# Kernel optimization log

Measured on AMD Instinct MI355X. Metric: run time of the kernel, lower is better.

The kernel has to match this reference:

```python
import jax, jax.numpy as jnp
import numpy as np

# Lens/CCD constants from the source module
DX = 0.00859375
F = 8.0
OX = 5.5 / 2.0   # CCD_width / 2
OY = 7.7 / 2.0   # CCD_length / 2

B, C, H, W = 4, 3, 1024, 2048


def _make_bn(h, w):
    # bn[i, j] = floor((cos(atan(dx*(j-ox)/f)) - 1) * (i - oy)), as in __init__
    j = np.arange(w, dtype=np.float64)
    i = np.arange(h, dtype=np.float64)
    a0 = np.arctan(DX * (j - OX) / F)
    bn = np.floor((np.cos(a0)[None, :] - 1.0) * (i[:, None] - OY))
    return bn.astype(np.int32)


def setup_inputs() -> dict:
    key = jax.random.key(0)
    k1, k2 = jax.random.split(key)
    x = jax.random.normal(k1, (B, C, H, W), dtype=jnp.float32)
    # Conv2d(3, 3, kernel_size=3, bias=False) weight: (out_c, in_c, kh, kw)
    weight = jax.random.normal(k2, (3, 3, 3, 3), dtype=jnp.float32) * 0.1
    bn = jnp.asarray(_make_bn(H, W))  # int32 distortion LUT, shape (H, W)
    return {"x": x, "weight": weight, "bn": bn}


def reference(x, weight, bn):
    B_, C_, H_, W_ = x.shape
    Hi, Wj = H_ - 2, W_ // 2 - 2  # active region: i+2 < H and j+2 < W//2
    i = jnp.arange(Hi)
    j = jnp.arange(Wj)
    p = jnp.arange(3)  # k // 3 (patch row)
    q = jnp.arange(3)  # k % 3  (patch col)
    # column used for the LUT wraps for j >= 256 (j1 = j % 256)
    j1 = jnp.where(j >= 256, j % 256, j)
    rows = i[:, None] + p[None, :]        # (Hi, 3)
    cols = j1[:, None] + q[None, :]       # (Wj, 3)
    # tb(i, j, p, q) = i + p + bn[i + p, j1 + q]
    bn_sel = bn[rows[:, None, :, None], cols[None, :, None, :]]  # (Hi, Wj, 3, 3)
    R = rows[:, None, :, None] + bn_sel                          # source row indices
    # Faithful quirk from the source: patch column index into input is q (0..2),
    # NOT j + q: matrix1[:, :, p, q] = input[:, :, tb, q]
    gathered = x[:, :, R, q]  # (B, C, Hi, Wj, 3, 3)
    out_act = jnp.einsum('bcijpq,ocpq->boij', gathered, weight)  # per-pixel 3x3 conv
    # guard from the source: only write when i + 2 + bn[i+2, j+2] < H
    mask = (i[:, None] + 2 + bn[i[:, None] + 2, j[None, :] + 2]) < H_
    out_act = out_act * mask.astype(out_act.dtype)
    return jnp.zeros((B_, C_, H_, W_), x.dtype).at[:, :, :Hi, :Wj].set(out_act)
```

## Files before the change

kernel.cpp:

```cpp
#include <hip/hip_runtime.h>


#define HH 1024
#define WW 2048
#define HI 1022
#define WJ 1022

__global__ __launch_bounds__(256, 4) void dis_conv_kernel(
    const float* __restrict__ x,
    const float* __restrict__ w,
    const int*   __restrict__ bn,
    float*       __restrict__ out)
{
    const int bi = blockIdx.x;
    const int b  = bi >> 10;
    const int i  = bi & 1023;
    const int t  = threadIdx.x;

    __shared__ __align__(16) float v[3][256];
    __shared__ __align__(16) float mask_s[1024];

    const bool activeRow = (i < HI);

    float acc0 = 0.f, acc1 = 0.f, acc2 = 0.f;
    if (activeRow) {
        const int jm = t;
        #pragma unroll
        for (int p = 0; p < 3; ++p) {
            const int r = i + p;
            const int* bnrow = bn + (size_t)r * WW;
            #pragma unroll
            for (int q = 0; q < 3; ++q) {
                int Rv = r + bnrow[jm + q];
                if (Rv < 0) Rv += HH;
                const float* xp = x + ((size_t)b * 3) * HH * WW + (size_t)Rv * WW + q;
                #pragma unroll
                for (int c = 0; c < 3; ++c) {
                    const float xv = xp[(size_t)c * HH * WW];
                    acc0 += xv * w[ 0 + c * 9 + p * 3 + q];
                    acc1 += xv * w[27 + c * 9 + p * 3 + q];
                    acc2 += xv * w[54 + c * 9 + p * 3 + q];
                }
            }
        }
    }
    v[0][t] = acc0;
    v[1][t] = acc1;
    v[2][t] = acc2;

    #pragma unroll
    for (int jj = 0; jj < 4; ++jj) {
        const int j = t + jj * 256;
        float m = 0.f;
        if (activeRow && j < WJ) {
            m = ((i + 2) + bn[(size_t)(i + 2) * WW + (j + 2)] < HH) ? 1.f : 0.f;
        }
        mask_s[j] = m;
    }
    __syncthreads();

    #pragma unroll
    for (int o = 0; o < 3; ++o) {
        float* orow = out + (((size_t)b * 3 + o) * HH + i) * WW;
        #pragma unroll
        for (int it = 0; it < 2; ++it) {
            const int j4 = (t + it * 256) * 4;
            float4 val;
            if (j4 < 1024) {
                const float4 vv = *(const float4*)&v[o][j4 & 255];
                const float4 mm = *(const float4*)&mask_s[j4];
                val = make_float4(vv.x * mm.x, vv.y * mm.y, vv.z * mm.z, vv.w * mm.w);
            } else {
                val = make_float4(0.f, 0.f, 0.f, 0.f);
            }
            *(float4*)&orow[j4] = val;
        }
    }
}

extern "C" void kernel_launch(void* const* d_in, const int* in_sizes, int n_in,
                              void* d_out, int out_size, void* d_ws, size_t ws_size,
                              hipStream_t stream) {
    const float* x   = (const float*)d_in[0];
    const float* w   = (const float*)d_in[1];
    const int*   bn  = (const int*)d_in[2];
    float*       out = (float*)d_out;

    dis_conv_kernel<<<dim3(4096), dim3(256), 0, stream>>>(x, w, bn, out);
}
```

Measured before the change: 176.7 us.

## Split into compute and write kernels, sharing LUT indices across batch

Computes the 256 distinct column values per row once in a first kernel that loads the bn LUT once and reuses it across all four batches, storing results and the mask in workspace. A second kernel then streams the masked values and zeros into the output with float4 stores. This removes the redundant per-batch bn reads and mask computation. In exchange it adds a second launch and a workspace round trip, and the compute kernel runs only 1022 blocks.

```diff
diff --git a/kernel.cpp b/kernel.cpp
--- a/kernel.cpp
+++ b/kernel.cpp
@@ -6,74 +6,102 @@
 #define HI 1022
 #define WJ 1022
 
-__global__ __launch_bounds__(256, 4) void dis_conv_kernel(
+#define VWS_FLOATS (12 * 1024 * 256)
+
+__global__ __launch_bounds__(256) void compute_v_kernel(
     const float* __restrict__ x,
     const float* __restrict__ w,
     const int*   __restrict__ bn,
+    float*       __restrict__ ws)
+{
+    const int i  = blockIdx.x;
+    const int jm = threadIdx.x;
+
+    int Rv[3][3];
+    #pragma unroll
+    for (int p = 0; p < 3; ++p) {
+        const int r = i + p;
+        const int* bnrow = bn + (size_t)r * WW;
+        #pragma unroll
+        for (int q = 0; q < 3; ++q) {
+            int rv = r + bnrow[jm + q];
+            if (rv < 0) rv += HH;
+            Rv[p][q] = rv;
+        }
+    }
+
+    float acc[4][3];
+    #pragma unroll
+    for (int b = 0; b < 4; ++b)
+        #pragma unroll
+        for (int o = 0; o < 3; ++o)
+            acc[b][o] = 0.f;
+
+    #pragma unroll
+    for (int b = 0; b < 4; ++b) {
+        #pragma unroll
+        for (int c = 0; c < 3; ++c) {
+            const float* xbase = x + (size_t)(b * 3 + c) * (HH * WW);
+            #pragma unroll
+            for (int p = 0; p < 3; ++p) {
+                #pragma unroll
+                for (int q = 0; q < 3; ++q) {
+                    const float xv = xbase[(size_t)Rv[p][q] * WW + q];
+                    #pragma unroll
+                    for (int o = 0; o < 3; ++o)
+                        acc[b][o] += xv * w[(o * 3 + c) * 9 + p * 3 + q];
+                }
+            }
+        }
+    }
+
+    #pragma unroll
+    for (int b = 0; b < 4; ++b)
+        #pragma unroll
+        for (int o = 0; o < 3; ++o)
+            ws[((size_t)(b * 3 + o) * HH + i) * 256 + jm] = acc[b][o];
+
+    float* mws = ws + VWS_FLOATS;
+    const int* bnm = bn + (size_t)(i + 2) * WW;
+    #pragma unroll
+    for (int k = 0; k < 4; ++k) {
+        const int j = jm + 256 * k;
+        float m = 0.f;
+        if (j < WJ)
+            m = ((i + 2) + bnm[j + 2] < HH) ? 1.f : 0.f;
+        mws[(size_t)i * 1024 + j] = m;
+    }
+}
+
+__global__ __launch_bounds__(256) void write_kernel(
+    const float* __restrict__ ws,
     float*       __restrict__ out)
 {
     const int bi = blockIdx.x;
     const int b  = bi >> 10;
     const int i  = bi & 1023;
-    const int t  = threadIdx.x;
+    const int j4 = threadIdx.x * 4;
 
-    __shared__ __align__(16) float v[3][256];
-    __shared__ __align__(16) float mask_s[1024];
+    const float4 z = make_float4(0.f, 0.f, 0.f, 0.f);
 
-    const bool activeRow = (i < HI);
-
-    float acc0 = 0.f, acc1 = 0.f, acc2 = 0.f;
-    if (activeRow) {
-        const int jm = t;
+    if (i < HI) {
+        const float* mrow = ws + VWS_FLOATS + (size_t)i * 1024;
+        const float4 mm = *(const float4*)&mrow[j4];
         #pragma unroll
-        for (int p = 0; p < 3; ++p) {
-            const int r = i + p;
-            const int* bnrow = bn + (size_t)r * WW;
-            #pragma unroll
-            for (int q = 0; q < 3; ++q) {
-                int Rv = r + bnrow[jm + q];
-                if (Rv < 0) Rv += HH;
-                const float* xp = x + ((size_t)b * 3) * HH * WW + (size_t)Rv * WW + q;
-                #pragma unroll
-                for (int c = 0; c < 3; ++c) {
-                    const float xv = xp[(size_t)c * HH * WW];
-                    acc0 += xv * w[ 0 + c * 9 + p * 3 + q];
-                    acc1 += xv * w[27 + c * 9 + p * 3 + q];
-                    acc2 += xv * w[54 + c * 9 + p * 3 + q];
-                }
-            }
+        for (int o = 0; o < 3; ++o) {
+            const float* vrow = ws + ((size_t)(b * 3 + o) * HH + i) * 256;
+            const float4 vv = *(const float4*)&vrow[j4 & 255];
+            float* orow = out + ((size_t)(b * 3 + o) * HH + i) * WW;
+            *(float4*)&orow[j4] = make_float4(vv.x * mm.x, vv.y * mm.y,
+                                              vv.z * mm.z, vv.w * mm.w);
+            *(float4*)&orow[j4 + 1024] = z;
         }
-    }
-    v[0][t] = acc0;
-    v[1][t] = acc1;
-    v[2][t] = acc2;
-
-    #pragma unroll
-    for (int jj = 0; jj < 4; ++jj) {
-        const int j = t + jj * 256;
-        float m = 0.f;
-        if (activeRow && j < WJ) {
-            m = ((i + 2) + bn[(size_t)(i + 2) * WW + (j + 2)] < HH) ? 1.f : 0.f;
-        }
-        mask_s[j] = m;
-    }
-    __syncthreads();
-
-    #pragma unroll
-    for (int o = 0; o < 3; ++o) {
-        float* orow = out + (((size_t)b * 3 + o) * HH + i) * WW;
+    } else {
         #pragma unroll
-        for (int it = 0; it < 2; ++it) {
-            const int j4 = (t + it * 256) * 4;
-            float4 val;
-            if (j4 < 1024) {
-                const float4 vv = *(const float4*)&v[o][j4 & 255];
-                const float4 mm = *(const float4*)&mask_s[j4];
-                val = make_float4(vv.x * mm.x, vv.y * mm.y, vv.z * mm.z, vv.w * mm.w);
-            } else {
-                val = make_float4(0.f, 0.f, 0.f, 0.f);
-            }
-            *(float4*)&orow[j4] = val;
+        for (int o = 0; o < 3; ++o) {
+            float* orow = out + ((size_t)(b * 3 + o) * HH + i) * WW;
+            *(float4*)&orow[j4]        = z;
+            *(float4*)&orow[j4 + 1024] = z;
         }
     }
 }
@@ -85,6 +113,8 @@
     const float* w   = (const float*)d_in[1];
     const int*   bn  = (const int*)d_in[2];
     float*       out = (float*)d_out;
+    float*       ws  = (float*)d_ws;
 
-    dis_conv_kernel<<<dim3(4096), dim3(256), 0, stream>>>(x, w, bn, out);
+    compute_v_kernel<<<dim3(HI), dim3(256), 0, stream>>>(x, w, bn, ws);
+    write_kernel<<<dim3(4096), dim3(256), 0, stream>>>(ws, out);
 }
```

Result: slower. 190.4 us (+7.8%).
